# Kernel tuning notes

Hardware: AMD Instinct MI355X
Metric: run time of the kernel (lower is better)

The kernel has to match this reference:

```python
import jax, jax.numpy as jnp
import numpy as np

N_NODES = 50000
N_EDGES = 600000
N_GRAPHS = 256
N_FL1, N_MPL, N_FL2, N_FL3 = 128, 128, 128, 64
EPS = 1e-12


def _glorot(key, shape):
    lim = float(np.sqrt(6.0 / (shape[0] + shape[1])))
    return jax.random.uniform(key, shape, jnp.float32, -lim, lim)


def setup_inputs() -> dict:
    key = jax.random.key(0)
    ks = jax.random.split(key, 16)
    x = jax.random.normal(ks[0], (N_NODES, 5), jnp.float32)
    edge_index = jax.random.randint(ks[1], (2, N_EDGES), 0, N_NODES, jnp.int64)
    batch = jnp.sort(jax.random.randint(ks[2], (N_NODES,), 0, N_GRAPHS, jnp.int64))
    return {
        "x": x,
        "edge_index": edge_index,
        "batch": batch,
        "W_pre": _glorot(ks[3], (5, N_FL1)),
        "b_pre": jnp.zeros((N_FL1,), jnp.float32),
        "W1_l": _glorot(ks[4], (N_FL1, N_MPL)),
        "b1": jnp.zeros((N_MPL,), jnp.float32),
        "W1_r": _glorot(ks[5], (N_FL1, N_MPL)),
        "W2_l": _glorot(ks[6], (N_MPL, N_MPL)),
        "b2": jnp.zeros((N_MPL,), jnp.float32),
        "W2_r": _glorot(ks[7], (N_MPL, N_MPL)),
        "W_p1": _glorot(ks[8], (N_MPL, N_FL2)),
        "b_p1": jnp.zeros((N_FL2,), jnp.float32),
        "W_p2": _glorot(ks[9], (N_FL2, N_FL3)),
        "b_p2": jnp.zeros((N_FL3,), jnp.float32),
        "W_out": _glorot(ks[10], (N_FL3, 1)),
        "b_out": jnp.zeros((1,), jnp.float32),
    }


def _sage_conv(x, src, dst, deg_inv, W_l, b_l, W_r):
    # mean-aggregate neighbor messages x[src] onto dst, then linear transforms
    agg = jax.ops.segment_sum(x[src], dst, num_segments=N_NODES) * deg_inv  # [N, d]
    out = agg @ W_l + b_l + x @ W_r
    # normalize=True -> L2 normalize per node (PyG F.normalize, eps=1e-12)
    norm = jnp.sqrt(jnp.sum(out * out, axis=-1, keepdims=True))
    return out / jnp.maximum(norm, EPS)


def reference(x, edge_index, batch, W_pre, b_pre, W1_l, b1, W1_r,
              W2_l, b2, W2_r, W_p1, b_p1, W_p2, b_p2, W_out, b_out):
    src, dst = edge_index[0], edge_index[1]
    deg = jax.ops.segment_sum(jnp.ones((N_EDGES,), jnp.float32), dst, num_segments=N_NODES)
    deg_inv = (1.0 / jnp.maximum(deg, 1.0))[:, None]

    h = jax.nn.relu(x @ W_pre + b_pre)
    h = jax.nn.relu(_sage_conv(h, src, dst, deg_inv, W1_l, b1, W1_r))
    h = jax.nn.relu(_sage_conv(h, src, dst, deg_inv, W2_l, b2, W2_r))

    # global_mean_pool over graph ids in batch
    g_sum = jax.ops.segment_sum(h, batch, num_segments=N_GRAPHS)  # [G, d]
    g_cnt = jax.ops.segment_sum(jnp.ones((N_NODES,), jnp.float32), batch, num_segments=N_GRAPHS)
    g = g_sum / jnp.maximum(g_cnt, 1.0)[:, None]

    g = jax.nn.relu(g @ W_p1 + b_p1)
    g = jax.nn.relu(g @ W_p2 + b_p2)
    return g @ W_out + b_out  # [G, 1]
```

## Files before the change

### kernel.cpp

```cpp
#include <hip/hip_runtime.h>
#include <hip/hip_bf16.h>

#define N_NODES 50000
#define N_EDGES 600000
#define N_GRAPHS 256
#define D 128
#define NTILES 1563

typedef __bf16 bf16x8 __attribute__((ext_vector_type(8)));
typedef float f32x16 __attribute__((ext_vector_type(16)));
typedef unsigned short u16x8 __attribute__((ext_vector_type(8)));

__device__ __forceinline__ float bf2f(unsigned short u) {
    unsigned v = ((unsigned)u) << 16;
    return __builtin_bit_cast(float, v);
}
__device__ __forceinline__ unsigned short f2bf(float f) {
    unsigned x = __builtin_bit_cast(unsigned, f);
    unsigned r = (x + 0x7fffu + ((x >> 16) & 1u)) >> 16;
    return (unsigned short)r;
}


#define ZERO_N (50048 + 32768)
#define ZERO_BLOCKS 324
#define PACK_BLOCKS 256
#define PRE_BLOCKS 3125

__global__ __launch_bounds__(256) void init_kernel(
    int* __restrict__ deg_gsum,
    const float* __restrict__ Wl1, const float* __restrict__ Wr1,
    const float* __restrict__ Wl2, const float* __restrict__ Wr2,
    unsigned short* __restrict__ Wpk,
    const float* __restrict__ x, const float* __restrict__ Wpre,
    const float* __restrict__ bpre, unsigned short* __restrict__ h0) {
    int bb = blockIdx.x;
    if (bb < ZERO_BLOCKS) {
        int i = bb * 256 + threadIdx.x;
        if (i < ZERO_N) deg_gsum[i] = 0;
    } else if (bb < ZERO_BLOCKS + PACK_BLOCKS) {
        int tid = (bb - ZERO_BLOCKS) * 256 + threadIdx.x;
        int conv = tid >> 15;
        int e = tid & 32767;
        int j = e & 7, lane = (e >> 3) & 63, ct = (e >> 9) & 3, kt = e >> 11;
        int k = kt * 16 + (lane >> 5) * 8 + j;
        int col = ct * 32 + (lane & 31);
        const float* Wl = conv ? Wl2 : Wl1;
        const float* Wr = conv ? Wr2 : Wr1;
        float v = (k < 128) ? Wl[k * 128 + col] : Wr[(k - 128) * 128 + col];
        Wpk[tid] = f2bf(v);
    } else {
        int idx = (bb - ZERO_BLOCKS - PACK_BLOCKS) * 256 + threadIdx.x;
        if (idx >= N_NODES * 16) return;
        int node = idx >> 4, j8 = (idx & 15) * 8;
        const float* xr = x + node * 5;
        float acc[8];
#pragma unroll
        for (int c = 0; c < 8; ++c) acc[c] = bpre[j8 + c];
#pragma unroll
        for (int k = 0; k < 5; ++k) {
            float xv = xr[k];
#pragma unroll
            for (int c = 0; c < 8; ++c) acc[c] += xv * Wpre[k * D + j8 + c];
        }
        u16x8 o;
#pragma unroll
        for (int c = 0; c < 8; ++c) o[c] = f2bf(fmaxf(acc[c], 0.f));
        *(u16x8*)&h0[(size_t)node * D + j8] = o;
    }
}


__global__ void deg_kernel(const int* __restrict__ dst, int* __restrict__ deg) {
    int e = blockIdx.x * 256 + threadIdx.x;
    if (e < N_EDGES) atomicAdd(&deg[dst[e]], 1);
}

__global__ __launch_bounds__(1024) void scan_blk_kernel(const int* __restrict__ deg,
                                                        int* __restrict__ partial,
                                                        int* __restrict__ bsum) {
    __shared__ int tmp[1024];
    int tid = threadIdx.x;
    int i = blockIdx.x * 1024 + tid;
    int v = (i < N_NODES) ? deg[i] : 0;
    tmp[tid] = v;
    __syncthreads();
    for (int off = 1; off < 1024; off <<= 1) {
        int add = (tid >= off) ? tmp[tid - off] : 0;
        __syncthreads();
        tmp[tid] += add;
        __syncthreads();
    }
    if (i < N_NODES) partial[i] = tmp[tid] - v;
    if (tid == 1023) bsum[blockIdx.x] = tmp[tid];
}

__global__ __launch_bounds__(256) void scan_fix_kernel(const int* __restrict__ partial,
                                                       const int* __restrict__ bsum,
                                                       const int* __restrict__ deg,
                                                       int* __restrict__ row_start,
                                                       int* __restrict__ cursor,
                                                       float* __restrict__ deg_inv) {
    __shared__ int boff_s;
    int bucket = (blockIdx.x * 256) >> 10;
    if (threadIdx.x < 64) {
        int l = threadIdx.x;
        int v = (l < bucket) ? bsum[l] : 0;
#pragma unroll
        for (int m = 32; m >= 1; m >>= 1) v += __shfl_xor(v, m);
        if (l == 0) boff_s = v;
    }
    __syncthreads();
    int i = blockIdx.x * 256 + threadIdx.x;
    if (i >= N_NODES) return;
    int dg = deg[i];
    int rs = partial[i] + boff_s;
    row_start[i] = rs;
    cursor[i] = rs;
    deg_inv[i] = 1.0f / fmaxf((float)dg, 1.0f);
    if (i == N_NODES - 1) row_start[N_NODES] = rs + dg;
}

__global__ void fill_kernel(const int* __restrict__ src, const int* __restrict__ dst,
                            int* __restrict__ cursor, int* __restrict__ csr_src) {
    int e = blockIdx.x * 256 + threadIdx.x;
    if (e < N_EDGES) {
        int slot = atomicAdd(&cursor[dst[e]], 1);
        csr_src[slot] = src[e];
    }
}


__global__ __launch_bounds__(256) void agg_kernel(const unsigned short* __restrict__ h,
                                                  const int* __restrict__ row_start,
                                                  const int* __restrict__ csr_src,
                                                  const float* __restrict__ deg_inv,
                                                  unsigned short* __restrict__ aggb) {
    int node = blockIdx.x * 16 + (threadIdx.x >> 4);
    int fl = threadIdx.x & 15;
    if (node >= N_NODES) return;
    int s = row_start[node], e = row_start[node + 1];
    float a[8] = {0.f, 0.f, 0.f, 0.f, 0.f, 0.f, 0.f, 0.f};
    int i = s;
    for (; i + 7 < e; i += 8) {
        int c[8];
#pragma unroll
        for (int q = 0; q < 8; ++q) c[q] = csr_src[i + q];
        bf16x8 v[8];
#pragma unroll
        for (int q = 0; q < 8; ++q) v[q] = *(const bf16x8*)(h + (size_t)c[q] * D + fl * 8);
#pragma unroll
        for (int q = 0; q < 8; ++q)
#pragma unroll
            for (int j = 0; j < 8; ++j) a[j] += (float)v[q][j];
    }
    for (; i + 3 < e; i += 4) {
        int c[4];
#pragma unroll
        for (int q = 0; q < 4; ++q) c[q] = csr_src[i + q];
        bf16x8 v[4];
#pragma unroll
        for (int q = 0; q < 4; ++q) v[q] = *(const bf16x8*)(h + (size_t)c[q] * D + fl * 8);
#pragma unroll
        for (int q = 0; q < 4; ++q)
#pragma unroll
            for (int j = 0; j < 8; ++j) a[j] += (float)v[q][j];
    }
    for (; i < e; ++i) {
        int c0 = csr_src[i];
        bf16x8 v0 = *(const bf16x8*)(h + (size_t)c0 * D + fl * 8);
#pragma unroll
        for (int j = 0; j < 8; ++j) a[j] += (float)v0[j];
    }
    float di = deg_inv[node];
    u16x8 o;
#pragma unroll
    for (int j = 0; j < 8; ++j) o[j] = f2bf(a[j] * di);
    *(u16x8*)(aggb + (size_t)node * D + fl * 8) = o;
}


__global__ __launch_bounds__(256) void lin_quad_kernel(const unsigned short* __restrict__ hin,
                                                       const unsigned short* __restrict__ aggb,
                                                       const unsigned short* __restrict__ Wp,
                                                       const float* __restrict__ b,
                                                       unsigned short* __restrict__ hout) {
    __shared__ float ssp[32][4];
    int t = threadIdx.x;
    int w = t >> 6;
    int lane = t & 63;
    int l31 = lane & 31, hi = lane >> 5;
    int row0 = blockIdx.x * 32;
    int rowg = row0 + l31;
    int rowc = (rowg < N_NODES) ? rowg : (N_NODES - 1);

    const unsigned short* arow = aggb + (size_t)rowc * D + hi * 8;
    const unsigned short* hrow = hin + (size_t)rowc * D + hi * 8;
    const unsigned short* wbase = Wp + (size_t)w * 512 + lane * 8;

    f32x16 acc = (f32x16)(0.0f);
#pragma unroll
    for (int kt = 0; kt < 16; ++kt) {
        const unsigned short* asrc = (kt < 8) ? (arow + kt * 16) : (hrow + (kt - 8) * 16);
        bf16x8 af = *(const bf16x8*)asrc;
        bf16x8 bfrag = *(const bf16x8*)(wbase + kt * 2048);
        acc = __builtin_amdgcn_mfma_f32_32x32x16_bf16(af, bfrag, acc, 0, 0, 0);
    }

    float bb = b[w * 32 + l31];

#pragma unroll
    for (int r = 0; r < 16; ++r) {
        float v = acc[r] + bb;
        float ss = v * v;
        ss += __shfl_xor(ss, 1);
        ss += __shfl_xor(ss, 2);
        ss += __shfl_xor(ss, 4);
        ss += __shfl_xor(ss, 8);
        ss += __shfl_xor(ss, 16);
        if (l31 == 0) ssp[(r & 3) + 8 * (r >> 2) + 4 * hi][w] = ss;
    }
    __syncthreads();

#pragma unroll
    for (int r = 0; r < 16; ++r) {
        int rl = (r & 3) + 8 * (r >> 2) + 4 * hi;
        float ss = ssp[rl][0] + ssp[rl][1] + ssp[rl][2] + ssp[rl][3];
        float sc = 1.0f / fmaxf(sqrtf(ss), 1e-12f);
        int row = row0 + rl;
        if (row < N_NODES) {
            float v = (acc[r] + bb) * sc;
            hout[(size_t)row * D + w * 32 + l31] = f2bf(fmaxf(v, 0.f));
        }
    }
}


__global__ __launch_bounds__(128) void pool_sum_kernel(const unsigned short* __restrict__ h,
                                                       const int* __restrict__ batch,
                                                       float* __restrict__ gsum) {
    int j = threadIdx.x;
    int i0 = blockIdx.x * 128;
    int i1 = i0 + 128;
    if (i1 > N_NODES) i1 = N_NODES;
    __shared__ int bids[128];
    if (i0 + j < N_NODES) bids[j] = batch[i0 + j];
    __syncthreads();
    float acc = 0.f;
    int cur = bids[0];
    for (int i = i0; i < i1; ++i) {
        int bid = bids[i - i0];
        if (bid != cur) {
            atomicAdd(&gsum[cur * D + j], acc);
            acc = 0.f;
            cur = bid;
        }
        acc += bf2f(h[(size_t)i * D + j]);
    }
    atomicAdd(&gsum[cur * D + j], acc);
}


__global__ __launch_bounds__(128) void mlp_kernel(const float* __restrict__ gsum,
                                                  const int* __restrict__ batch,
                                                  const float* __restrict__ Wp1,
                                                  const float* __restrict__ bp1,
                                                  const float* __restrict__ Wp2,
                                                  const float* __restrict__ bp2,
                                                  const float* __restrict__ Wout,
                                                  const float* __restrict__ bout,
                                                  float* __restrict__ out) {
    __shared__ float gin[128], y1[128], y2[64];
    __shared__ float cnt_s;
    int gid = blockIdx.x, j = threadIdx.x;
    if (j == 0) {
        int lo = 0, hi = N_NODES;
        while (lo < hi) { int m = (lo + hi) >> 1; if (batch[m] < gid) lo = m + 1; else hi = m; }
        int start = lo;
        lo = start; hi = N_NODES;
        while (lo < hi) { int m = (lo + hi) >> 1; if (batch[m] < gid + 1) lo = m + 1; else hi = m; }
        cnt_s = fmaxf((float)(lo - start), 1.0f);
    }
    __syncthreads();
    gin[j] = gsum[gid * 128 + j] / cnt_s;
    __syncthreads();
    float a = bp1[j];
    for (int k = 0; k < 128; ++k) a += gin[k] * Wp1[k * 128 + j];
    y1[j] = fmaxf(a, 0.f);
    __syncthreads();
    if (j < 64) {
        float a2 = bp2[j];
        for (int k = 0; k < 128; ++k) a2 += y1[k] * Wp2[k * 64 + j];
        y2[j] = fmaxf(a2, 0.f);
    }
    __syncthreads();
    if (j < 64) {
        float v = y2[j] * Wout[j];
#pragma unroll
        for (int m = 32; m >= 1; m >>= 1) v += __shfl_xor(v, m);
        if (j == 0) out[gid] = v + bout[0];
    }
}


extern "C" void kernel_launch(void* const* d_in, const int* in_sizes, int n_in,
                              void* d_out, int out_size, void* d_ws, size_t ws_size,
                              hipStream_t stream) {
    const float* x     = (const float*)d_in[0];
    const int*   ei    = (const int*)d_in[1];
    const int*   batch = (const int*)d_in[2];
    const float* W_pre = (const float*)d_in[3];
    const float* b_pre = (const float*)d_in[4];
    const float* W1_l  = (const float*)d_in[5];
    const float* b1    = (const float*)d_in[6];
    const float* W1_r  = (const float*)d_in[7];
    const float* W2_l  = (const float*)d_in[8];
    const float* b2    = (const float*)d_in[9];
    const float* W2_r  = (const float*)d_in[10];
    const float* W_p1  = (const float*)d_in[11];
    const float* b_p1  = (const float*)d_in[12];
    const float* W_p2  = (const float*)d_in[13];
    const float* b_p2  = (const float*)d_in[14];
    const float* W_out = (const float*)d_in[15];
    const float* b_out = (const float*)d_in[16];

    const int* src = ei;
    const int* dst = ei + N_EDGES;

    size_t off = 0;
    auto carve = [&](size_t bytes) {
        void* p = (char*)d_ws + off;
        off += (bytes + 255) & ~(size_t)255;
        return p;
    };
    int* deg       = (int*)carve(50048 * 4 + 32768 * 4);
    float* gsum    = (float*)(deg + 50048);
    int* row_start = (int*)carve((N_NODES + 1) * 4);
    int* cursor    = (int*)carve(N_NODES * 4);
    int* csr_src   = (int*)carve(N_EDGES * 4);
    float* deg_inv = (float*)carve(N_NODES * 4);
    int* partial   = (int*)carve(N_NODES * 4);
    int* bsum      = (int*)carve(64 * 4);
    unsigned short* h0   = (unsigned short*)carve((size_t)N_NODES * D * 2);
    unsigned short* h1   = (unsigned short*)carve((size_t)N_NODES * D * 2);
    unsigned short* aggb = (unsigned short*)carve((size_t)N_NODES * D * 2);
    unsigned short* Wp   = (unsigned short*)carve(65536 * 2);
    unsigned short* h2 = h0;
    float* out = (float*)d_out;

    const int nblk_scan = (N_NODES + 1023) / 1024;

    init_kernel<<<ZERO_BLOCKS + PACK_BLOCKS + PRE_BLOCKS, 256, 0, stream>>>(
        deg, W1_l, W1_r, W2_l, W2_r, Wp, x, W_pre, b_pre, h0);

    deg_kernel<<<(N_EDGES + 255) / 256, 256, 0, stream>>>(dst, deg);
    scan_blk_kernel<<<nblk_scan, 1024, 0, stream>>>(deg, partial, bsum);
    scan_fix_kernel<<<(N_NODES + 255) / 256, 256, 0, stream>>>(partial, bsum, deg,
                                                               row_start, cursor, deg_inv);
    fill_kernel<<<(N_EDGES + 255) / 256, 256, 0, stream>>>(src, dst, cursor, csr_src);

    agg_kernel<<<(N_NODES + 15) / 16, 256, 0, stream>>>(h0, row_start, csr_src, deg_inv, aggb);
    lin_quad_kernel<<<NTILES, 256, 0, stream>>>(h0, aggb, Wp, b1, h1);

    agg_kernel<<<(N_NODES + 15) / 16, 256, 0, stream>>>(h1, row_start, csr_src, deg_inv, aggb);
    lin_quad_kernel<<<NTILES, 256, 0, stream>>>(h1, aggb, Wp + 32768, b2, h2);

    pool_sum_kernel<<<(N_NODES + 127) / 128, 128, 0, stream>>>(h2, batch, gsum);
    mlp_kernel<<<N_GRAPHS, 128, 0, stream>>>(gsum, batch, W_p1, b_p1, W_p2, b_p2,
                                             W_out, b_out, out);
}
```

Measured before the change: 228.6 us.

## Compute full 32x128 tile per single wave in linear layer, drop LDS reduction

Measured after the change: 212.9 us. 6.8% less time.

```diff
diff --git a/kernel.cpp b/kernel.cpp
--- a/kernel.cpp
+++ b/kernel.cpp
@@ -10,6 +10,7 @@
 typedef __bf16 bf16x8 __attribute__((ext_vector_type(8)));
 typedef float f32x16 __attribute__((ext_vector_type(16)));
 typedef unsigned short u16x8 __attribute__((ext_vector_type(8)));
+typedef unsigned short u16x4 __attribute__((ext_vector_type(4)));
 
 __device__ __forceinline__ float bf2f(unsigned short u) {
     unsigned v = ((unsigned)u) << 16;
@@ -44,7 +45,7 @@
         int e = tid & 32767;
         int j = e & 7, lane = (e >> 3) & 63, ct = (e >> 9) & 3, kt = e >> 11;
         int k = kt * 16 + (lane >> 5) * 8 + j;
-        int col = ct * 32 + (lane & 31);
+        int col = (lane & 31) * 4 + ct;
         const float* Wl = conv ? Wl2 : Wl1;
         const float* Wr = conv ? Wr2 : Wr1;
         float v = (k < 128) ? Wl[k * 128 + col] : Wr[(k - 128) * 128 + col];
@@ -180,57 +181,61 @@
 }
 
 
-__global__ __launch_bounds__(256) void lin_quad_kernel(const unsigned short* __restrict__ hin,
-                                                       const unsigned short* __restrict__ aggb,
-                                                       const unsigned short* __restrict__ Wp,
-                                                       const float* __restrict__ b,
-                                                       unsigned short* __restrict__ hout) {
-    __shared__ float ssp[32][4];
-    int t = threadIdx.x;
-    int w = t >> 6;
-    int lane = t & 63;
+__global__ __launch_bounds__(64) void lin_mfma_kernel(const unsigned short* __restrict__ hin,
+                                                      const unsigned short* __restrict__ aggb,
+                                                      const unsigned short* __restrict__ Wp,
+                                                      const float* __restrict__ b,
+                                                      unsigned short* __restrict__ hout) {
+    int wg = blockIdx.x;
+    int lane = threadIdx.x;
     int l31 = lane & 31, hi = lane >> 5;
-    int row0 = blockIdx.x * 32;
+    int row0 = wg * 32;
     int rowg = row0 + l31;
-    int rowc = (rowg < N_NODES) ? rowg : (N_NODES - 1);
-
-    const unsigned short* arow = aggb + (size_t)rowc * D + hi * 8;
-    const unsigned short* hrow = hin + (size_t)rowc * D + hi * 8;
-    const unsigned short* wbase = Wp + (size_t)w * 512 + lane * 8;
-
-    f32x16 acc = (f32x16)(0.0f);
+    if (rowg > N_NODES - 1) rowg = N_NODES - 1;
+
+    const unsigned short* arow = aggb + (size_t)rowg * D + hi * 8;
+    const unsigned short* hrow = hin + (size_t)rowg * D + hi * 8;
+    const unsigned short* wbase = Wp + lane * 8;
+
+    f32x16 acc[4];
+#pragma unroll
+    for (int ct = 0; ct < 4; ++ct) acc[ct] = (f32x16)(0.0f);
+
 #pragma unroll
     for (int kt = 0; kt < 16; ++kt) {
         const unsigned short* asrc = (kt < 8) ? (arow + kt * 16) : (hrow + (kt - 8) * 16);
         bf16x8 af = *(const bf16x8*)asrc;
-        bf16x8 bfrag = *(const bf16x8*)(wbase + kt * 2048);
-        acc = __builtin_amdgcn_mfma_f32_32x32x16_bf16(af, bfrag, acc, 0, 0, 0);
-    }
-
-    float bb = b[w * 32 + l31];
+#pragma unroll
+        for (int ct = 0; ct < 4; ++ct) {
+            bf16x8 bfrag = *(const bf16x8*)(wbase + (kt * 4 + ct) * 512);
+            acc[ct] = __builtin_amdgcn_mfma_f32_32x32x16_bf16(af, bfrag, acc[ct], 0, 0, 0);
+        }
+    }
+
+    float4 b4 = *(const float4*)&b[l31 * 4];
+    float bb[4] = {b4.x, b4.y, b4.z, b4.w};
 
 #pragma unroll
     for (int r = 0; r < 16; ++r) {
-        float v = acc[r] + bb;
-        float ss = v * v;
+        float v[4];
+        float ss = 0.f;
+#pragma unroll
+        for (int ct = 0; ct < 4; ++ct) {
+            v[ct] = acc[ct][r] + bb[ct];
+            ss += v[ct] * v[ct];
+        }
         ss += __shfl_xor(ss, 1);
         ss += __shfl_xor(ss, 2);
         ss += __shfl_xor(ss, 4);
         ss += __shfl_xor(ss, 8);
         ss += __shfl_xor(ss, 16);
-        if (l31 == 0) ssp[(r & 3) + 8 * (r >> 2) + 4 * hi][w] = ss;
-    }
-    __syncthreads();
-
-#pragma unroll
-    for (int r = 0; r < 16; ++r) {
-        int rl = (r & 3) + 8 * (r >> 2) + 4 * hi;
-        float ss = ssp[rl][0] + ssp[rl][1] + ssp[rl][2] + ssp[rl][3];
         float sc = 1.0f / fmaxf(sqrtf(ss), 1e-12f);
-        int row = row0 + rl;
+        int row = row0 + (r & 3) + 8 * (r >> 2) + 4 * hi;
         if (row < N_NODES) {
-            float v = (acc[r] + bb) * sc;
-            hout[(size_t)row * D + w * 32 + l31] = f2bf(fmaxf(v, 0.f));
+            u16x4 o;
+#pragma unroll
+            for (int ct = 0; ct < 4; ++ct) o[ct] = f2bf(fmaxf(v[ct] * sc, 0.f));
+            *(u16x4*)(hout + (size_t)row * D + l31 * 4) = o;
         }
     }
 }
@@ -360,10 +365,10 @@
     fill_kernel<<<(N_EDGES + 255) / 256, 256, 0, stream>>>(src, dst, cursor, csr_src);
 
     agg_kernel<<<(N_NODES + 15) / 16, 256, 0, stream>>>(h0, row_start, csr_src, deg_inv, aggb);
-    lin_quad_kernel<<<NTILES, 256, 0, stream>>>(h0, aggb, Wp, b1, h1);
+    lin_mfma_kernel<<<NTILES, 64, 0, stream>>>(h0, aggb, Wp, b1, h1);
 
     agg_kernel<<<(N_NODES + 15) / 16, 256, 0, stream>>>(h1, row_start, csr_src, deg_inv, aggb);
-    lin_quad_kernel<<<NTILES, 256, 0, stream>>>(h1, aggb, Wp + 32768, b2, h2);
+    lin_mfma_kernel<<<NTILES, 64, 0, stream>>>(h1, aggb, Wp + 32768, b2, h2);
 
     pool_sum_kernel<<<(N_NODES + 127) / 128, 128, 0, stream>>>(h2, batch, gsum);
     mlp_kernel<<<N_GRAPHS, 128, 0, stream>>>(gsum, batch, W_p1, b_p1, W_p2, b_p2,
```
